# Kernel tuning notes

Measured on AMD Instinct MI355X. Metric: run time of the kernel, lower is better.

Reference implementation:

```python
import jax, jax.numpy as jnp
import numpy as np

EXTENT = 1.0  # kernel-point influence radius (init kwarg 'extent')
B, N, M, H, K, F, C = 4, 16384, 16384, 32, 15, 64, 64


def setup_inputs() -> dict:
    key = jax.random.key(0)
    ks = jax.random.split(key, 6)
    points = jax.random.uniform(ks[0], (B, N, 3), dtype=jnp.float32)
    features = jax.random.normal(ks[1], (B, N, F), dtype=jnp.float32)
    output_points = jax.random.uniform(ks[2], (B, M, 3), dtype=jnp.float32)
    neighbor_indices = jax.random.randint(ks[3], (B, M, H), 0, N)
    # kernel point dispositions inside a ball of radius 1.5*extent (load_kernels stand-in)
    k_points = jax.random.uniform(ks[4], (K, 3), minval=-1.0, maxval=1.0, dtype=jnp.float32) * (1.5 * EXTENT) / jnp.sqrt(3.0)
    k_values = jax.random.normal(ks[5], (K, F, C), dtype=jnp.float32) * 0.05
    return {
        'points': points, 'features': features, 'output_points': output_points,
        'k_points': k_points, 'k_values': k_values, 'neighbor_indices': neighbor_indices,
    }


def reference(points, features, output_points, k_points, k_values, neighbor_indices):
    b, m, h = neighbor_indices.shape
    idx = neighbor_indices.reshape(b, m * h, 1)
    # batched gather (tf.gather batch_dims=1)
    neigh_pts = jnp.take_along_axis(points, idx, axis=1).reshape(b, m, h, 3)
    neigh_feat = jnp.take_along_axis(features, idx, axis=1).reshape(b, m, h, -1)
    # relative coords to each output point, then to each kernel point
    rel = neigh_pts - output_points[:, :, None, :]                # [B,M,H,3]
    diff = rel[:, :, :, None, :] - k_points                       # [B,M,H,K,3]
    sq_d = jnp.sum(diff * diff, axis=-1)                          # [B,M,H,K]
    # linear influence
    w = jnp.maximum(1.0 - jnp.sqrt(sq_d) / EXTENT, 0.0)           # [B,M,H,K]
    # weight neighbor features per kernel point, then apply per-kernel linear map, sum over K
    wf = jnp.einsum('bmhk,bmhf->bmkf', w, neigh_feat)             # [B,M,K,F]
    out = jnp.einsum('bmkf,kfc->bmc', wf, k_values)               # [B,M,C]
    return out
```

## Files before the change

kernel.cpp:

```cpp
#include <hip/hip_runtime.h>

#define BATCH 4
#define NPTS 16384
#define MPTS 16384
#define NH 32
#define NK 15
#define NF 64
#define NC 64

typedef short short8 __attribute__((ext_vector_type(8)));
typedef float floatx4 __attribute__((ext_vector_type(4)));

__device__ __forceinline__ unsigned short f2bf(float x) {
    unsigned int u = __builtin_bit_cast(unsigned int, x);
    u = u + 0x7FFFu + ((u >> 16) & 1u);
    return (unsigned short)(u >> 16);
}

__device__ __forceinline__ unsigned pack_trunc(float lo, float hi) {
    return __builtin_amdgcn_perm(__builtin_bit_cast(unsigned, hi),
                                 __builtin_bit_cast(unsigned, lo), 0x07060302u);
}

__global__ void prep_kernel(const float* __restrict__ kv, const float* __restrict__ feat,
                            unsigned short* __restrict__ vp, unsigned short* __restrict__ featbf) {
    if (blockIdx.x < 32) {
        const int gid = blockIdx.x * 256 + threadIdx.x;
        const int lane = gid & 63;
        const int ct   = (gid >> 6) & 3;
        const int kk   = gid >> 8;
        const int c    = ct * 16 + (lane & 15);
        const int kap0 = kk * 32 + (lane >> 4) * 8;
        unsigned int o[4];
        #pragma unroll
        for (int jj = 0; jj < 4; jj++) {
            unsigned short lo, hi;
            {
                const int kap = kap0 + jj * 2;
                const int f = kap >> 4, k = kap & 15;
                lo = (k < NK) ? f2bf(kv[((size_t)(k * NF + f)) * NC + c]) : (unsigned short)0;
            }
            {
                const int kap = kap0 + jj * 2 + 1;
                const int f = kap >> 4, k = kap & 15;
                hi = (k < NK) ? f2bf(kv[((size_t)(k * NF + f)) * NC + c]) : (unsigned short)0;
            }
            o[jj] = (unsigned)lo | ((unsigned)hi << 16);
        }
        *(uint4*)(vp + (size_t)gid * 8) = make_uint4(o[0], o[1], o[2], o[3]);
    } else {
        const int gid = (blockIdx.x - 32) * 256 + threadIdx.x;
        const size_t base = (size_t)gid * 8;
        float4 a = *(const float4*)(feat + base);
        float4 b = *(const float4*)(feat + base + 4);
        uint4 o;
        o.x = (unsigned)f2bf(a.x) | ((unsigned)f2bf(a.y) << 16);
        o.y = (unsigned)f2bf(a.z) | ((unsigned)f2bf(a.w) << 16);
        o.z = (unsigned)f2bf(b.x) | ((unsigned)f2bf(b.y) << 16);
        o.w = (unsigned)f2bf(b.z) | ((unsigned)f2bf(b.w) << 16);
        *(uint4*)(featbf + base) = o;
    }
}

__global__ __launch_bounds__(256, 5) void kpconv_kernel(
    const float* __restrict__ points,
    const unsigned short* __restrict__ featbf,
    const float* __restrict__ outpts,
    const float* __restrict__ kpts,
    const unsigned short* __restrict__ vp,
    const int*   __restrict__ nbr,
    float* __restrict__ out)
{
    __shared__ __align__(16) unsigned short awf[16 * 512];
    __shared__ __align__(16) unsigned short feat_s[4 * 1160];
    __shared__ int   idx_s[512];
    __shared__ float opt_s[48];
    __shared__ float kp_s[48];

    const int tid   = threadIdx.x;
    const int batch = blockIdx.x & 3;
    const int m0    = (blockIdx.x >> 2) << 4;

    if (tid < 48) kp_s[tid] = (tid < 45) ? kpts[tid] : 1e9f;
    if (tid >= 64 && tid < 112)
        opt_s[tid - 64] = outpts[(size_t)(batch * MPTS + m0) * 3 + (tid - 64)];
    {
        const size_t nb = (size_t)(batch * MPTS + m0) * NH;
        idx_s[tid]       = nbr[nb + tid];
        idx_s[256 + tid] = nbr[nb + 256 + tid];
    }
    __syncthreads();

    const int g    = tid >> 6;
    const int lane = tid & 63;
    const int cl   = lane & 15;
    const int q    = lane >> 4;
    const int sa   = cl;
    const int sfc  = q;

    const unsigned short* fbase = featbf + (size_t)(batch * NPTS) * NF;

    uint4 praA, prbA, praB, prbB;
    {
        const int srow0 = (0 * 4 + g) * 32 + sa * 2;
        const int ida0 = idx_s[srow0], idb0 = idx_s[srow0 + 1];
        praA = *(const uint4*)(fbase + (size_t)ida0 * NF + sfc * 8);
        prbA = *(const uint4*)(fbase + (size_t)idb0 * NF + sfc * 8);
        const int srow1 = (1 * 4 + g) * 32 + sa * 2;
        const int ida1 = idx_s[srow1], idb1 = idx_s[srow1 + 1];
        praB = *(const uint4*)(fbase + (size_t)ida1 * NF + sfc * 8);
        prbB = *(const uint4*)(fbase + (size_t)idb1 * NF + sfc * 8);
    }

    float4* rel4 = (float4*)awf;
    #pragma unroll
    for (int rr = 0; rr < 2; rr++) {
        const int row = tid * 2 + rr;
        const int id  = idx_s[row];
        const int pm  = row >> 5;
        const float* pp = points + ((size_t)(batch * NPTS) + id) * 3;
        rel4[row + (row >> 3)] = make_float4(pp[0] - opt_s[pm * 3 + 0],
                                             pp[1] - opt_s[pm * 3 + 1],
                                             pp[2] - opt_s[pm * 3 + 2], 0.f);
    }
    __syncthreads();

    short8 af[4];
    {
        const float kx = kp_s[cl * 3 + 0];
        const float ky = kp_s[cl * 3 + 1];
        const float kz = kp_s[cl * 3 + 2];
        #pragma unroll
        for (int rp = 0; rp < 4; rp++) {
            const int p = rp * 4 + g;
            float wv[8];
            #pragma unroll
            for (int j = 0; j < 8; j++) {
                const float4 rr = rel4[36 * p + 9 * q + j];
                const float dx = rr.x - kx, dy = rr.y - ky, dz = rr.z - kz;
                const float d2 = dx * dx + dy * dy + dz * dz;
                wv[j] = fmaxf(1.f - __builtin_amdgcn_sqrtf(d2), 0.f);
            }
            uint4 ua;
            ua.x = pack_trunc(wv[0], wv[1]);
            ua.y = pack_trunc(wv[2], wv[3]);
            ua.z = pack_trunc(wv[4], wv[5]);
            ua.w = pack_trunc(wv[6], wv[7]);
            af[rp] = __builtin_bit_cast(short8, ua);
        }
    }
    __syncthreads();

    floatx4 acc0 = {0.f, 0.f, 0.f, 0.f};
    floatx4 acc1 = {0.f, 0.f, 0.f, 0.f};
    const unsigned short* vpg = vp + g * 512 + lane * 8;
    unsigned short* dp = &feat_s[g * 1160 + sfc * 288 + sa * 2];

    #pragma unroll
    for (int it = 0; it < 8; it++) {
        const int r  = it & 3;
        const int p  = r * 4 + g;

        *(unsigned*)(dp + 0 * 36) = __builtin_amdgcn_perm(prbA.x, praA.x, 0x05040100u);
        *(unsigned*)(dp + 1 * 36) = __builtin_amdgcn_perm(prbA.x, praA.x, 0x07060302u);
        *(unsigned*)(dp + 2 * 36) = __builtin_amdgcn_perm(prbA.y, praA.y, 0x05040100u);
        *(unsigned*)(dp + 3 * 36) = __builtin_amdgcn_perm(prbA.y, praA.y, 0x07060302u);
        *(unsigned*)(dp + 4 * 36) = __builtin_amdgcn_perm(prbA.z, praA.z, 0x05040100u);
        *(unsigned*)(dp + 5 * 36) = __builtin_amdgcn_perm(prbA.z, praA.z, 0x07060302u);
        *(unsigned*)(dp + 6 * 36) = __builtin_amdgcn_perm(prbA.w, praA.w, 0x05040100u);
        *(unsigned*)(dp + 7 * 36) = __builtin_amdgcn_perm(prbA.w, praA.w, 0x07060302u);

        praA = praB; prbA = prbB;
        if (it < 6) {
            const int nit = it + 2;
            const int nfh = nit >> 2, nr = nit & 3;
            const int srow = (nr * 4 + g) * 32 + sa * 2;
            const int id0 = idx_s[srow], id1 = idx_s[srow + 1];
            praB = *(const uint4*)(fbase + (size_t)id0 * NF + nfh * 32 + sfc * 8);
            prbB = *(const uint4*)(fbase + (size_t)id1 * NF + nfh * 32 + sfc * 8);
        }

        #pragma unroll
        for (int t = 0; t < 2; t++) {
            const uint4 ub = *(const uint4*)&feat_s[g * 1160 + (t * 16 + cl) * 36 + q * 8];
            floatx4 dd = {0.f, 0.f, 0.f, 0.f};
            dd = __builtin_amdgcn_mfma_f32_16x16x32_bf16(af[r], __builtin_bit_cast(short8, ub), dd, 0, 0, 0);
            const int kk    = 8 * t + (cl >> 1);
            const int q2    = (2 * cl + (q >> 1)) & 3;
            const int chunk = (p ^ kk) | (q2 << 4);
            unsigned* wp = (unsigned*)awf + kk * 256 + chunk * 4 + (q & 1) * 2;
            wp[0] = pack_trunc(dd[0], dd[1]);
            wp[1] = pack_trunc(dd[2], dd[3]);
        }

        if (it == 3) {
            __syncthreads();
            #pragma unroll 4
            for (int kk = 0; kk < 16; kk++) {
                const int chunk = (cl ^ kk) | (lane & 48);
                const uint4 uA = *(const uint4*)&awf[kk * 512 + chunk * 8];
                const uint4 uB = *(const uint4*)(vpg + (size_t)kk * 2048);
                if (kk & 1)
                    acc1 = __builtin_amdgcn_mfma_f32_16x16x32_bf16(
                        __builtin_bit_cast(short8, uA), __builtin_bit_cast(short8, uB), acc1, 0, 0, 0);
                else
                    acc0 = __builtin_amdgcn_mfma_f32_16x16x32_bf16(
                        __builtin_bit_cast(short8, uA), __builtin_bit_cast(short8, uB), acc0, 0, 0, 0);
            }
            __syncthreads();
        }
    }

    __syncthreads();
    #pragma unroll 4
    for (int kk = 0; kk < 16; kk++) {
        const int chunk = (cl ^ kk) | (lane & 48);
        const uint4 uA = *(const uint4*)&awf[kk * 512 + chunk * 8];
        const uint4 uB = *(const uint4*)(vpg + (size_t)(16 + kk) * 2048);
        if (kk & 1)
            acc1 = __builtin_amdgcn_mfma_f32_16x16x32_bf16(
                __builtin_bit_cast(short8, uA), __builtin_bit_cast(short8, uB), acc1, 0, 0, 0);
        else
            acc0 = __builtin_amdgcn_mfma_f32_16x16x32_bf16(
                __builtin_bit_cast(short8, uA), __builtin_bit_cast(short8, uB), acc0, 0, 0, 0);
    }

    __syncthreads();
    float* ob = (float*)awf;
    #pragma unroll
    for (int ri = 0; ri < 4; ri++)
        ob[(q * 4 + ri) * 68 + g * 16 + cl] = acc0[ri] + acc1[ri];
    __syncthreads();
    {
        const int row = tid >> 4;
        const int c4  = tid & 15;
        const floatx4 v = *(const floatx4*)&ob[row * 68 + c4 * 4];
        floatx4* dst = (floatx4*)&out[((size_t)(batch * MPTS + m0 + row)) * NC + c4 * 4];
        __builtin_nontemporal_store(v, dst);
    }
}

extern "C" void kernel_launch(void* const* d_in, const int* in_sizes, int n_in,
                              void* d_out, int out_size, void* d_ws, size_t ws_size,
                              hipStream_t stream) {
    const float* points   = (const float*)d_in[0];
    const float* features = (const float*)d_in[1];
    const float* outpts   = (const float*)d_in[2];
    const float* kpts     = (const float*)d_in[3];
    const float* kvals    = (const float*)d_in[4];
    const int*   nbr      = (const int*)d_in[5];
    float* out = (float*)d_out;

    unsigned short* vp     = (unsigned short*)d_ws;
    unsigned short* featbf = (unsigned short*)((char*)d_ws + 131072);

    prep_kernel<<<2080, 256, 0, stream>>>(kvals, features, vp, featbf);

    const int blocks = BATCH * (MPTS / 16);
    kpconv_kernel<<<blocks, 256, 0, stream>>>(points, featbf, outpts, kpts, vp, nbr, out);
}
```

Measured before the change: 136.5 us.

## Prefetch kernel-weight fragments before barrier, shrink index smem, raise occupancy

Loads the first eight global weight fragments into registers before each barrier and refills the ring during the MFMA loop, so global latency overlaps the sync and matrix work. It raises the MFMA loop's wave priority and fully unrolls it. Neighbor indices are stored as 16-bit values in shared memory and loaded as int2, and launch bounds go from 5 to 6 waves per EU. Register pressure from the 8-entry uint4 ring together with the tighter launch bound may cause spills.

Result: slower. 181.2 us (+32.7%).

```diff
diff --git a/kernel.cpp b/kernel.cpp
--- a/kernel.cpp
+++ b/kernel.cpp
@@ -62,7 +62,7 @@
     }
 }
 
-__global__ __launch_bounds__(256, 5) void kpconv_kernel(
+__global__ __launch_bounds__(256, 6) void kpconv_kernel(
     const float* __restrict__ points,
     const unsigned short* __restrict__ featbf,
     const float* __restrict__ outpts,
@@ -73,7 +73,7 @@
 {
     __shared__ __align__(16) unsigned short awf[16 * 512];
     __shared__ __align__(16) unsigned short feat_s[4 * 1160];
-    __shared__ int   idx_s[512];
+    __shared__ __align__(8) unsigned short idx_s[512];
     __shared__ float opt_s[48];
     __shared__ float kp_s[48];
 
@@ -86,8 +86,9 @@
         opt_s[tid - 64] = outpts[(size_t)(batch * MPTS + m0) * 3 + (tid - 64)];
     {
         const size_t nb = (size_t)(batch * MPTS + m0) * NH;
-        idx_s[tid]       = nbr[nb + tid];
-        idx_s[256 + tid] = nbr[nb + 256 + tid];
+        const int2 nn = *(const int2*)(nbr + nb + tid * 2);
+        *(unsigned*)&idx_s[tid * 2] =
+            (unsigned)(unsigned short)nn.x | ((unsigned)(unsigned short)nn.y << 16);
     }
     __syncthreads();
 
@@ -194,12 +195,19 @@
         }
 
         if (it == 3) {
+            uint4 vb[8];
+            #pragma unroll
+            for (int j = 0; j < 8; j++)
+                vb[j] = *(const uint4*)(vpg + (size_t)j * 2048);
             __syncthreads();
-            #pragma unroll 4
+            __builtin_amdgcn_s_setprio(1);
+            #pragma unroll
             for (int kk = 0; kk < 16; kk++) {
                 const int chunk = (cl ^ kk) | (lane & 48);
                 const uint4 uA = *(const uint4*)&awf[kk * 512 + chunk * 8];
-                const uint4 uB = *(const uint4*)(vpg + (size_t)kk * 2048);
+                const uint4 uB = vb[kk & 7];
+                if (kk < 8)
+                    vb[kk & 7] = *(const uint4*)(vpg + (size_t)(kk + 8) * 2048);
                 if (kk & 1)
                     acc1 = __builtin_amdgcn_mfma_f32_16x16x32_bf16(
                         __builtin_bit_cast(short8, uA), __builtin_bit_cast(short8, uB), acc1, 0, 0, 0);
@@ -207,22 +215,33 @@
                     acc0 = __builtin_amdgcn_mfma_f32_16x16x32_bf16(
                         __builtin_bit_cast(short8, uA), __builtin_bit_cast(short8, uB), acc0, 0, 0, 0);
             }
+            __builtin_amdgcn_s_setprio(0);
             __syncthreads();
         }
     }
 
-    __syncthreads();
-    #pragma unroll 4
-    for (int kk = 0; kk < 16; kk++) {
-        const int chunk = (cl ^ kk) | (lane & 48);
-        const uint4 uA = *(const uint4*)&awf[kk * 512 + chunk * 8];
-        const uint4 uB = *(const uint4*)(vpg + (size_t)(16 + kk) * 2048);
-        if (kk & 1)
-            acc1 = __builtin_amdgcn_mfma_f32_16x16x32_bf16(
-                __builtin_bit_cast(short8, uA), __builtin_bit_cast(short8, uB), acc1, 0, 0, 0);
-        else
-            acc0 = __builtin_amdgcn_mfma_f32_16x16x32_bf16(
-                __builtin_bit_cast(short8, uA), __builtin_bit_cast(short8, uB), acc0, 0, 0, 0);
+    {
+        uint4 vb[8];
+        #pragma unroll
+        for (int j = 0; j < 8; j++)
+            vb[j] = *(const uint4*)(vpg + (size_t)(16 + j) * 2048);
+        __syncthreads();
+        __builtin_amdgcn_s_setprio(1);
+        #pragma unroll
+        for (int kk = 0; kk < 16; kk++) {
+            const int chunk = (cl ^ kk) | (lane & 48);
+            const uint4 uA = *(const uint4*)&awf[kk * 512 + chunk * 8];
+            const uint4 uB = vb[kk & 7];
+            if (kk < 8)
+                vb[kk & 7] = *(const uint4*)(vpg + (size_t)(24 + kk) * 2048);
+            if (kk & 1)
+                acc1 = __builtin_amdgcn_mfma_f32_16x16x32_bf16(
+                    __builtin_bit_cast(short8, uA), __builtin_bit_cast(short8, uB), acc1, 0, 0, 0);
+            else
+                acc0 = __builtin_amdgcn_mfma_f32_16x16x32_bf16(
+                    __builtin_bit_cast(short8, uA), __builtin_bit_cast(short8, uB), acc0, 0, 0, 0);
+        }
+        __builtin_amdgcn_s_setprio(0);
     }
 
     __syncthreads();
```

## Run two 16-point tiles per 512-thread block in a staggered phase pipeline

Applied to the files above, without the earlier changes.

Each block now handles 32 output points with two 256-thread halves that run the same phases offset by one step. While one half computes its kernel-point weights or the feature-weighting MFMAs, the other half gathers neighbours or runs the k_values GEMM, so memory gathers and MFMA work from different phases overlap inside the block. Neighbour indices are stored as 16-bit values in shared memory, kernel points and output points are read straight from global memory, and results are stored directly without a shared-memory transpose. s_setprio raises wave priority during the second GEMM. Risks are more barriers per block, lower occupancy from larger LDS use and 512-thread blocks, and less coalesced output stores.

New measurement: 139.3 us. 1.02x slower.

```diff
diff --git a/kernel.cpp b/kernel.cpp
--- a/kernel.cpp
+++ b/kernel.cpp
@@ -21,6 +21,17 @@
     return __builtin_amdgcn_perm(__builtin_bit_cast(unsigned, hi),
                                  __builtin_bit_cast(unsigned, lo), 0x07060302u);
 }
+
+#define STAGE_FEAT8(pa, pb) do {                                                  \
+    *(unsigned*)(dp + 0 * 36) = __builtin_amdgcn_perm((pb).x, (pa).x, 0x05040100u); \
+    *(unsigned*)(dp + 1 * 36) = __builtin_amdgcn_perm((pb).x, (pa).x, 0x07060302u); \
+    *(unsigned*)(dp + 2 * 36) = __builtin_amdgcn_perm((pb).y, (pa).y, 0x05040100u); \
+    *(unsigned*)(dp + 3 * 36) = __builtin_amdgcn_perm((pb).y, (pa).y, 0x07060302u); \
+    *(unsigned*)(dp + 4 * 36) = __builtin_amdgcn_perm((pb).z, (pa).z, 0x05040100u); \
+    *(unsigned*)(dp + 5 * 36) = __builtin_amdgcn_perm((pb).z, (pa).z, 0x07060302u); \
+    *(unsigned*)(dp + 6 * 36) = __builtin_amdgcn_perm((pb).w, (pa).w, 0x05040100u); \
+    *(unsigned*)(dp + 7 * 36) = __builtin_amdgcn_perm((pb).w, (pa).w, 0x07060302u); \
+} while (0)
 
 __global__ void prep_kernel(const float* __restrict__ kv, const float* __restrict__ feat,
                             unsigned short* __restrict__ vp, unsigned short* __restrict__ featbf) {
@@ -62,7 +73,7 @@
     }
 }
 
-__global__ __launch_bounds__(256, 5) void kpconv_kernel(
+__global__ __launch_bounds__(512, 4) void kpconv_kernel(
     const float* __restrict__ points,
     const unsigned short* __restrict__ featbf,
     const float* __restrict__ outpts,
@@ -71,27 +82,18 @@
     const int*   __restrict__ nbr,
     float* __restrict__ out)
 {
-    __shared__ __align__(16) unsigned short awf[16 * 512];
-    __shared__ __align__(16) unsigned short feat_s[4 * 1160];
-    __shared__ int   idx_s[512];
-    __shared__ float opt_s[48];
-    __shared__ float kp_s[48];
+    __shared__ __align__(16) unsigned short awf[2 * 8192];
+    __shared__ __align__(16) unsigned short feat_s[8 * 1160];
+    __shared__ __align__(8) unsigned short idx_s[2 * 512];
 
     const int tid   = threadIdx.x;
     const int batch = blockIdx.x & 3;
-    const int m0    = (blockIdx.x >> 2) << 4;
-
-    if (tid < 48) kp_s[tid] = (tid < 45) ? kpts[tid] : 1e9f;
-    if (tid >= 64 && tid < 112)
-        opt_s[tid - 64] = outpts[(size_t)(batch * MPTS + m0) * 3 + (tid - 64)];
-    {
-        const size_t nb = (size_t)(batch * MPTS + m0) * NH;
-        idx_s[tid]       = nbr[nb + tid];
-        idx_s[256 + tid] = nbr[nb + 256 + tid];
-    }
-    __syncthreads();
+    const int m0    = (blockIdx.x >> 2) << 5;
 
     const int g    = tid >> 6;
+    const int hb   = g >> 2;
+    const int gl   = g & 3;
+    const int tidh = tid & 255;
     const int lane = tid & 63;
     const int cl   = lane & 15;
     const int q    = lane >> 4;
@@ -99,145 +101,140 @@
     const int sfc  = q;
 
     const unsigned short* fbase = featbf + (size_t)(batch * NPTS) * NF;
+    const unsigned short* vpg   = vp + gl * 512 + lane * 8;
+    unsigned short* dp = &feat_s[g * 1160 + sfc * 288 + sa * 2];
 
     uint4 praA, prbA, praB, prbB;
-    {
-        const int srow0 = (0 * 4 + g) * 32 + sa * 2;
-        const int ida0 = idx_s[srow0], idb0 = idx_s[srow0 + 1];
-        praA = *(const uint4*)(fbase + (size_t)ida0 * NF + sfc * 8);
-        prbA = *(const uint4*)(fbase + (size_t)idb0 * NF + sfc * 8);
-        const int srow1 = (1 * 4 + g) * 32 + sa * 2;
-        const int ida1 = idx_s[srow1], idb1 = idx_s[srow1 + 1];
-        praB = *(const uint4*)(fbase + (size_t)ida1 * NF + sfc * 8);
-        prbB = *(const uint4*)(fbase + (size_t)idb1 * NF + sfc * 8);
-    }
-
-    float4* rel4 = (float4*)awf;
-    #pragma unroll
-    for (int rr = 0; rr < 2; rr++) {
-        const int row = tid * 2 + rr;
-        const int id  = idx_s[row];
-        const int pm  = row >> 5;
-        const float* pp = points + ((size_t)(batch * NPTS) + id) * 3;
-        rel4[row + (row >> 3)] = make_float4(pp[0] - opt_s[pm * 3 + 0],
-                                             pp[1] - opt_s[pm * 3 + 1],
-                                             pp[2] - opt_s[pm * 3 + 2], 0.f);
-    }
-    __syncthreads();
-
     short8 af[4];
-    {
-        const float kx = kp_s[cl * 3 + 0];
-        const float ky = kp_s[cl * 3 + 1];
-        const float kz = kp_s[cl * 3 + 2];
-        #pragma unroll
-        for (int rp = 0; rp < 4; rp++) {
-            const int p = rp * 4 + g;
-            float wv[8];
-            #pragma unroll
-            for (int j = 0; j < 8; j++) {
-                const float4 rr = rel4[36 * p + 9 * q + j];
-                const float dx = rr.x - kx, dy = rr.y - ky, dz = rr.z - kz;
-                const float d2 = dx * dx + dy * dy + dz * dz;
-                wv[j] = fmaxf(1.f - __builtin_amdgcn_sqrtf(d2), 0.f);
-            }
-            uint4 ua;
-            ua.x = pack_trunc(wv[0], wv[1]);
-            ua.y = pack_trunc(wv[2], wv[3]);
-            ua.z = pack_trunc(wv[4], wv[5]);
-            ua.w = pack_trunc(wv[6], wv[7]);
-            af[rp] = __builtin_bit_cast(short8, ua);
-        }
-    }
-    __syncthreads();
-
     floatx4 acc0 = {0.f, 0.f, 0.f, 0.f};
     floatx4 acc1 = {0.f, 0.f, 0.f, 0.f};
-    const unsigned short* vpg = vp + g * 512 + lane * 8;
-    unsigned short* dp = &feat_s[g * 1160 + sfc * 288 + sa * 2];
-
-    #pragma unroll
-    for (int it = 0; it < 8; it++) {
-        const int r  = it & 3;
-        const int p  = r * 4 + g;
-
-        *(unsigned*)(dp + 0 * 36) = __builtin_amdgcn_perm(prbA.x, praA.x, 0x05040100u);
-        *(unsigned*)(dp + 1 * 36) = __builtin_amdgcn_perm(prbA.x, praA.x, 0x07060302u);
-        *(unsigned*)(dp + 2 * 36) = __builtin_amdgcn_perm(prbA.y, praA.y, 0x05040100u);
-        *(unsigned*)(dp + 3 * 36) = __builtin_amdgcn_perm(prbA.y, praA.y, 0x07060302u);
-        *(unsigned*)(dp + 4 * 36) = __builtin_amdgcn_perm(prbA.z, praA.z, 0x05040100u);
-        *(unsigned*)(dp + 5 * 36) = __builtin_amdgcn_perm(prbA.z, praA.z, 0x07060302u);
-        *(unsigned*)(dp + 6 * 36) = __builtin_amdgcn_perm(prbA.w, praA.w, 0x05040100u);
-        *(unsigned*)(dp + 7 * 36) = __builtin_amdgcn_perm(prbA.w, praA.w, 0x07060302u);
-
-        praA = praB; prbA = prbB;
-        if (it < 6) {
-            const int nit = it + 2;
-            const int nfh = nit >> 2, nr = nit & 3;
-            const int srow = (nr * 4 + g) * 32 + sa * 2;
-            const int id0 = idx_s[srow], id1 = idx_s[srow + 1];
-            praB = *(const uint4*)(fbase + (size_t)id0 * NF + nfh * 32 + sfc * 8);
-            prbB = *(const uint4*)(fbase + (size_t)id1 * NF + nfh * 32 + sfc * 8);
-        }
-
-        #pragma unroll
-        for (int t = 0; t < 2; t++) {
-            const uint4 ub = *(const uint4*)&feat_s[g * 1160 + (t * 16 + cl) * 36 + q * 8];
-            floatx4 dd = {0.f, 0.f, 0.f, 0.f};
-            dd = __builtin_amdgcn_mfma_f32_16x16x32_bf16(af[r], __builtin_bit_cast(short8, ub), dd, 0, 0, 0);
-            const int kk    = 8 * t + (cl >> 1);
-            const int q2    = (2 * cl + (q >> 1)) & 3;
-            const int chunk = (p ^ kk) | (q2 << 4);
-            unsigned* wp = (unsigned*)awf + kk * 256 + chunk * 4 + (q & 1) * 2;
-            wp[0] = pack_trunc(dd[0], dd[1]);
-            wp[1] = pack_trunc(dd[2], dd[3]);
-        }
-
-        if (it == 3) {
-            __syncthreads();
-            #pragma unroll 4
-            for (int kk = 0; kk < 16; kk++) {
-                const int chunk = (cl ^ kk) | (lane & 48);
-                const uint4 uA = *(const uint4*)&awf[kk * 512 + chunk * 8];
-                const uint4 uB = *(const uint4*)(vpg + (size_t)kk * 2048);
-                if (kk & 1)
-                    acc1 = __builtin_amdgcn_mfma_f32_16x16x32_bf16(
-                        __builtin_bit_cast(short8, uA), __builtin_bit_cast(short8, uB), acc1, 0, 0, 0);
-                else
-                    acc0 = __builtin_amdgcn_mfma_f32_16x16x32_bf16(
-                        __builtin_bit_cast(short8, uA), __builtin_bit_cast(short8, uB), acc0, 0, 0, 0);
-            }
-            __syncthreads();
-        }
-    }
-
-    __syncthreads();
-    #pragma unroll 4
-    for (int kk = 0; kk < 16; kk++) {
-        const int chunk = (cl ^ kk) | (lane & 48);
-        const uint4 uA = *(const uint4*)&awf[kk * 512 + chunk * 8];
-        const uint4 uB = *(const uint4*)(vpg + (size_t)(16 + kk) * 2048);
-        if (kk & 1)
-            acc1 = __builtin_amdgcn_mfma_f32_16x16x32_bf16(
-                __builtin_bit_cast(short8, uA), __builtin_bit_cast(short8, uB), acc1, 0, 0, 0);
-        else
-            acc0 = __builtin_amdgcn_mfma_f32_16x16x32_bf16(
-                __builtin_bit_cast(short8, uA), __builtin_bit_cast(short8, uB), acc0, 0, 0, 0);
-    }
-
-    __syncthreads();
-    float* ob = (float*)awf;
-    #pragma unroll
-    for (int ri = 0; ri < 4; ri++)
-        ob[(q * 4 + ri) * 68 + g * 16 + cl] = acc0[ri] + acc1[ri];
-    __syncthreads();
-    {
-        const int row = tid >> 4;
-        const int c4  = tid & 15;
-        const floatx4 v = *(const floatx4*)&ob[row * 68 + c4 * 4];
-        floatx4* dst = (floatx4*)&out[((size_t)(batch * MPTS + m0 + row)) * NC + c4 * 4];
-        __builtin_nontemporal_store(v, dst);
-    }
+
+
+#define PH_P0(T) do {                                                              \
+    {                                                                              \
+        const size_t nb = (size_t)(batch * MPTS + m0 + (T) * 16) * NH;             \
+        const int2 nn = *(const int2*)(nbr + nb + tidh * 2);                       \
+        *(unsigned*)&idx_s[(T) * 512 + tidh * 2] =                                 \
+            (unsigned)(unsigned short)nn.x | ((unsigned)(unsigned short)nn.y << 16); \
+    }                                                                              \
+    float4* rel4 = (float4*)(awf + (T) * 8192);                                    \
+    const int pm = tidh >> 4;                                                      \
+    const float* ob3 = outpts + (size_t)(batch * MPTS + m0 + (T) * 16 + pm) * 3;   \
+    const float ox = ob3[0], oy = ob3[1], oz = ob3[2];                             \
+    _Pragma("unroll")                                                              \
+    for (int rr = 0; rr < 2; rr++) {                                               \
+        const int row = tidh * 2 + rr;                                             \
+        const int id  = idx_s[(T) * 512 + row];                                    \
+        const float* pp = points + ((size_t)(batch * NPTS) + id) * 3;              \
+        rel4[row + (row >> 3)] = make_float4(pp[0] - ox, pp[1] - oy, pp[2] - oz, 0.f); \
+    }                                                                              \
+} while (0)
+
+#define PH_P1(T) do {                                                              \
+    const float4* rel4 = (const float4*)(awf + (T) * 8192);                        \
+    const float kx = (cl < 15) ? kpts[cl * 3 + 0] : 1e9f;                          \
+    const float ky = (cl < 15) ? kpts[cl * 3 + 1] : 1e9f;                          \
+    const float kz = (cl < 15) ? kpts[cl * 3 + 2] : 1e9f;                          \
+    _Pragma("unroll")                                                              \
+    for (int rp = 0; rp < 4; rp++) {                                               \
+        const int p = rp * 4 + gl;                                                 \
+        float wv[8];                                                               \
+        _Pragma("unroll")                                                          \
+        for (int j = 0; j < 8; j++) {                                              \
+            const float4 rr = rel4[36 * p + 9 * q + j];                            \
+            const float dx = rr.x - kx, dy = rr.y - ky, dz = rr.z - kz;            \
+            const float d2 = dx * dx + dy * dy + dz * dz;                          \
+            wv[j] = fmaxf(1.f - __builtin_amdgcn_sqrtf(d2), 0.f);                  \
+        }                                                                          \
+        uint4 ua;                                                                  \
+        ua.x = pack_trunc(wv[0], wv[1]);                                           \
+        ua.y = pack_trunc(wv[2], wv[3]);                                           \
+        ua.z = pack_trunc(wv[4], wv[5]);                                           \
+        ua.w = pack_trunc(wv[6], wv[7]);                                           \
+        af[rp] = __builtin_bit_cast(short8, ua);                                   \
+    }                                                                              \
+    {                                                                              \
+        const int srow0 = (0 * 4 + gl) * 32 + sa * 2;                              \
+        const int ida0 = idx_s[(T) * 512 + srow0], idb0 = idx_s[(T) * 512 + srow0 + 1]; \
+        praA = *(const uint4*)(fbase + (size_t)ida0 * NF + sfc * 8);               \
+        prbA = *(const uint4*)(fbase + (size_t)idb0 * NF + sfc * 8);               \
+        const int srow1 = (1 * 4 + gl) * 32 + sa * 2;                              \
+        const int ida1 = idx_s[(T) * 512 + srow1], idb1 = idx_s[(T) * 512 + srow1 + 1]; \
+        praB = *(const uint4*)(fbase + (size_t)ida1 * NF + sfc * 8);               \
+        prbB = *(const uint4*)(fbase + (size_t)idb1 * NF + sfc * 8);               \
+    }                                                                              \
+} while (0)
+
+#define PH_E1(T, FH) do {                                                          \
+    _Pragma("unroll")                                                              \
+    for (int itl = 0; itl < 4; itl++) {                                            \
+        const int it = (FH) * 4 + itl;                                             \
+        const int r  = it & 3;                                                     \
+        const int p  = r * 4 + gl;                                                 \
+        STAGE_FEAT8(praA, prbA);                                                   \
+        praA = praB; prbA = prbB;                                                  \
+        if (it < 6) {                                                              \
+            const int nit = it + 2;                                                \
+            const int nfh = nit >> 2, nr = nit & 3;                                \
+            const int srow = (nr * 4 + gl) * 32 + sa * 2;                          \
+            const int id0 = idx_s[(T) * 512 + srow], id1 = idx_s[(T) * 512 + srow + 1]; \
+            praB = *(const uint4*)(fbase + (size_t)id0 * NF + nfh * 32 + sfc * 8); \
+            prbB = *(const uint4*)(fbase + (size_t)id1 * NF + nfh * 32 + sfc * 8); \
+        }                                                                          \
+        _Pragma("unroll")                                                          \
+        for (int t = 0; t < 2; t++) {                                              \
+            const uint4 ub = *(const uint4*)&feat_s[g * 1160 + (t * 16 + cl) * 36 + q * 8]; \
+            floatx4 dd = {0.f, 0.f, 0.f, 0.f};                                     \
+            dd = __builtin_amdgcn_mfma_f32_16x16x32_bf16(af[r], __builtin_bit_cast(short8, ub), dd, 0, 0, 0); \
+            const int kk    = 8 * t + (cl >> 1);                                   \
+            const int q2    = (2 * cl + (q >> 1)) & 3;                             \
+            const int chunk = (p ^ kk) | (q2 << 4);                                \
+            unsigned* wp = (unsigned*)(awf + (T) * 8192) + kk * 256 + chunk * 4 + (q & 1) * 2; \
+            wp[0] = pack_trunc(dd[0], dd[1]);                                      \
+            wp[1] = pack_trunc(dd[2], dd[3]);                                      \
+        }                                                                          \
+    }                                                                              \
+} while (0)
+
+#define PH_E2(T, HF) do {                                                          \
+    __builtin_amdgcn_s_setprio(1);                                                 \
+    _Pragma("unroll 4")                                                            \
+    for (int kk = 0; kk < 16; kk++) {                                              \
+        const int chunk = (cl ^ kk) | (lane & 48);                                 \
+        const uint4 uA = *(const uint4*)&awf[(T) * 8192 + kk * 512 + chunk * 8];   \
+        const uint4 uB = *(const uint4*)(vpg + (size_t)((HF) * 16 + kk) * 2048);   \
+        if (kk & 1)                                                                \
+            acc1 = __builtin_amdgcn_mfma_f32_16x16x32_bf16(                        \
+                __builtin_bit_cast(short8, uA), __builtin_bit_cast(short8, uB), acc1, 0, 0, 0); \
+        else                                                                       \
+            acc0 = __builtin_amdgcn_mfma_f32_16x16x32_bf16(                        \
+                __builtin_bit_cast(short8, uA), __builtin_bit_cast(short8, uB), acc0, 0, 0, 0); \
+    }                                                                              \
+    __builtin_amdgcn_s_setprio(0);                                                 \
+} while (0)
+
+#define PH_STORE(T) do {                                                           \
+    _Pragma("unroll")                                                              \
+    for (int ri = 0; ri < 4; ri++) {                                               \
+        const float v = acc0[ri] + acc1[ri];                                       \
+        __builtin_nontemporal_store(v,                                             \
+            &out[((size_t)(batch * MPTS + m0 + (T) * 16 + q * 4 + ri)) * NC + gl * 16 + cl]); \
+    }                                                                              \
+} while (0)
+
+    if (hb == 0) { PH_P0(0); }
+    __syncthreads();
+    if (hb == 0) { PH_P1(0); } else { PH_P0(1); }
+    __syncthreads();
+    if (hb == 0) { PH_E1(0, 0); } else { PH_P1(1); }
+    __syncthreads();
+    if (hb == 0) { PH_E2(0, 0); } else { PH_E1(1, 0); }
+    __syncthreads();
+    if (hb == 0) { PH_E1(0, 1); } else { PH_E2(1, 0); }
+    __syncthreads();
+    if (hb == 0) { PH_E2(0, 1); PH_STORE(0); } else { PH_E1(1, 1); }
+    __syncthreads();
+    if (hb == 1) { PH_E2(1, 1); PH_STORE(1); }
 }
 
 extern "C" void kernel_launch(void* const* d_in, const int* in_sizes, int n_in,
@@ -256,6 +253,6 @@
 
     prep_kernel<<<2080, 256, 0, stream>>>(kvals, features, vp, featbf);
 
-    const int blocks = BATCH * (MPTS / 16);
-    kpconv_kernel<<<blocks, 256, 0, stream>>>(points, featbf, outpts, kpts, vp, nbr, out);
-}
+    const int blocks = BATCH * (MPTS / 32);
+    kpconv_kernel<<<blocks, 512, 0, stream>>>(points, featbf, outpts, kpts, vp, nbr, out);
+}
```
